# Kernel optimization log

Measured on AMD Instinct MI355X. Metric: run time of the kernel, lower is better.

## Reference

```python
import jax, jax.numpy as jnp
import numpy as np

B, C, H, W = 16, 3, 512, 512
TH, TW = 32, 32  # template h, w


def setup_inputs() -> dict:
    key = jax.random.key(0)
    k1, k2 = jax.random.split(key)
    im = jax.random.normal(k1, (B, C, H, W), dtype=jnp.float32)
    template = jax.random.normal(k2, (B, C, TH, TW), dtype=jnp.float32)
    return {"im": im, "template": template}


def _integral(x):
    # double cumsum -> integral image
    return jnp.cumsum(jnp.cumsum(x, axis=-1), axis=-2)


def _rect_sum(int_im, out_h, out_w, rh, rw):
    # Sum over rh x rw rectangles centered on each pixel. Because the gather
    # indices in the torch code form contiguous ranges, advanced indexing
    # reduces to 4 static slices of the integral image.
    return (int_im[..., :out_h, :out_w] + int_im[..., rh:, rw:]
            - int_im[..., :out_h, rw:] - int_im[..., rh:, :out_w])


def _ncc(im, template):
    Hh, Ww = im.shape[-2], im.shape[-1]
    th, tw = template.shape[-2], template.shape[-1]
    padWl = (tw - 1) // 2
    padWr = padWl + 1 - tw % 2
    padHt = (th - 1) // 2
    padHb = padHt + 1 - th % 2
    rh = padHt + padHb + 1  # rectangle height (== th for even th)
    rw = padWl + padWr + 1
    pad2d = ((0, 0), (0, 0), (padHt + 1, padHb), (padWl + 1, padWr))

    # local-mean centering via integral image
    rect = _rect_sum(_integral(jnp.pad(im, pad2d)), Hh, Ww, rh, rw)
    im_c = im - rect / (th * tw)
    t_c = template - template.mean(axis=(-2, -1), keepdims=True)

    # local energy via second integral image over squared centered image
    rect2 = _rect_sum(_integral(jnp.pad(im_c * im_c, pad2d)), Hh, Ww, rh, rw)
    energy = jnp.sqrt(jnp.clip(rect2, 0.0))
    t_norm = jnp.sqrt(jnp.sum(t_c * t_c, axis=(-2, -1), keepdims=True))

    # FFT cross-correlation (padding='same')
    ph = Hh + th - th % 2 - Hh % 2
    pw = Ww + tw - tw % 2 - Ww % 2
    f_im = jnp.fft.rfft2(im_c / energy, s=(ph, pw))
    f_t = jnp.fft.rfft2(jnp.flip(t_c / t_norm, axis=(-2, -1)), s=(ph, pw))
    full = jnp.fft.irfft2(f_im * f_t, s=(ph, pw))
    hH, hW = th // 2, tw // 2
    return full[..., hH:hH + Hh, hW:hW + Ww]


def reference(im, template):
    return _ncc(im, template)
```

## Files before the change

### kernel.cpp

```cpp
#include <hip/hip_runtime.h>
#include <hip/hip_bf16.h>
#include <math.h>

#define HH 512
#define WW 512
#define BC 48
#define GW 544
#define GH 545
#define PST (GH * GW)

#define ROWB 384
#define COPYSTRIDE 6208
#define BUFSTRIDE (2 * COPYSTRIDE)
#define LDSBYTES (2 * BUFSTRIDE)

#define SIMS 98

typedef __bf16 v8bf __attribute__((ext_vector_type(8)));
typedef float v16f __attribute__((ext_vector_type(16)));

__global__ __launch_bounds__(256) void k_template(const float* __restrict__ t,
                                                  __hip_bfloat16* __restrict__ tn)
{
    __shared__ float red[256];
    const int bc = blockIdx.x, tid = threadIdx.x;
    const float* tp = t + bc * 1024;
    float v0 = tp[tid], v1 = tp[tid + 256], v2 = tp[tid + 512], v3 = tp[tid + 768];
    red[tid] = v0 + v1 + v2 + v3;
    __syncthreads();
    for (int sft = 128; sft > 0; sft >>= 1) {
        if (tid < sft) red[tid] += red[tid + sft];
        __syncthreads();
    }
    float mean = red[0] * (1.0f / 1024.0f);
    __syncthreads();
    float c0 = v0 - mean, c1 = v1 - mean, c2 = v2 - mean, c3 = v3 - mean;
    red[tid] = c0 * c0 + c1 * c1 + c2 * c2 + c3 * c3;
    __syncthreads();
    for (int sft = 128; sft > 0; sft >>= 1) {
        if (tid < sft) red[tid] += red[tid + sft];
        __syncthreads();
    }
    float norm = sqrtf(red[0]);
    __hip_bfloat16* o = tn + bc * 1024;
    o[tid] = __float2bfloat16(c0 / norm);
    o[tid + 256] = __float2bfloat16(c1 / norm);
    o[tid + 512] = __float2bfloat16(c2 / norm);
    o[tid + 768] = __float2bfloat16(c3 / norm);
}

__global__ __launch_bounds__(256) void k_center2(const float* __restrict__ im,
                                                 __hip_bfloat16* __restrict__ T0)
{
    __shared__ __hip_bfloat16 sim[159 * SIMS];
    __shared__ float hs[159 * 64];
    const int j0 = blockIdx.x * 64;
    const int i0 = blockIdx.y * 128;
    const int plane = blockIdx.z;
    const int tid = threadIdx.x;
    const size_t iplane = (size_t)plane * HH * WW;
    const size_t gplane = (size_t)plane * PST;

    for (int k = tid; k < 159 * 96; k += 256) {
        int r = k / 96, c = k - r * 96;
        int gi = i0 + r - 15, gj = j0 + c - 16;
        float v = (gi >= 0 && gi < HH && gj >= 0 && gj < WW)
                      ? im[iplane + (size_t)gi * WW + gj] : 0.f;
        sim[r * SIMS + c] = __float2bfloat16(v);
    }
    __syncthreads();

    if (tid < 159) {
        const __hip_bfloat16* sr = sim + tid * SIMS;
        float s0 = 0.f;
#pragma unroll
        for (int c = 1; c <= 32; c++) s0 += __bfloat162float(sr[c]);
        hs[tid * 64] = s0;
        for (int j = 1; j < 64; j++) {
            s0 += __bfloat162float(sr[j + 32]) - __bfloat162float(sr[j]);
            hs[tid * 64 + j] = s0;
        }
    }
    __syncthreads();

    const int tc = tid & 63;
    const int lr0 = (tid >> 6) * 32;
    float run = 0.f;
#pragma unroll
    for (int d = 0; d < 32; d++) run += hs[(lr0 + d) * 64 + tc];
    for (int rr = 0; rr < 32; rr++) {
        int lr = lr0 + rr;
        int gi = i0 + lr;
        float imv = __bfloat162float(sim[(lr + 15) * SIMS + tc + 16]);
        float val = imv - run * (1.0f / 1024.0f);
        T0[gplane + (size_t)(16 + gi) * GW + 16 + j0 + tc] = __float2bfloat16(val);
        if (rr < 31) run += hs[(lr + 32) * 64 + tc] - hs[lr * 64 + tc];
    }
    if (blockIdx.x == 0) {
        for (int k = tid; k < 128 * 16; k += 256) {
            int rr = k >> 4, x = k & 15;
            T0[gplane + (size_t)(16 + i0 + rr) * GW + x] = __float2bfloat16(0.f);
        }
    }
    if (blockIdx.x == 7) {
        for (int k = tid; k < 128 * 16; k += 256) {
            int rr = k >> 4, x = k & 15;
            T0[gplane + (size_t)(16 + i0 + rr) * GW + 528 + x] = __float2bfloat16(0.f);
        }
    }
    if (blockIdx.x == 0 && blockIdx.y == 0) {
        for (int k = tid; k < 16 * GW; k += 256)
            T0[gplane + k] = __float2bfloat16(0.f);
    }
    if (blockIdx.x == 0 && blockIdx.y == 3) {
        size_t b = gplane + (size_t)528 * GW;
        for (int k = tid; k < 17 * GW; k += 256)
            T0[b + k] = __float2bfloat16(0.f);
    }
}

__global__ __launch_bounds__(256) void k_norm2(const __hip_bfloat16* __restrict__ T0,
                                               __hip_bfloat16* __restrict__ G0,
                                               __hip_bfloat16* __restrict__ G1)
{
    __shared__ __hip_bfloat16 sim[159 * SIMS];
    __shared__ float hs[159 * 64];
    const int j0 = blockIdx.x * 64;
    const int i0 = blockIdx.y * 128;
    const int plane = blockIdx.z;
    const int tid = threadIdx.x;
    const size_t gplane = (size_t)plane * PST;

    for (int k = tid; k < 159 * 96; k += 256) {
        int r = k / 96, c = k - r * 96;
        sim[r * SIMS + c] = T0[gplane + (size_t)(i0 + 1 + r) * GW + j0 + c];
    }
    __syncthreads();

    if (tid < 159) {
        const __hip_bfloat16* sr = sim + tid * SIMS;
        float s0 = 0.f;
#pragma unroll
        for (int c = 1; c <= 32; c++) {
            float v = __bfloat162float(sr[c]);
            s0 += v * v;
        }
        hs[tid * 64] = s0;
        for (int j = 1; j < 64; j++) {
            float a = __bfloat162float(sr[j + 32]);
            float b = __bfloat162float(sr[j]);
            s0 += a * a - b * b;
            hs[tid * 64 + j] = s0;
        }
    }
    __syncthreads();

    const int tc = tid & 63;
    const int lr0 = (tid >> 6) * 32;
    float run = 0.f;
#pragma unroll
    for (int d = 0; d < 32; d++) run += hs[(lr0 + d) * 64 + tc];
    for (int rr = 0; rr < 32; rr++) {
        int lr = lr0 + rr;
        int gi = i0 + lr;
        int c = j0 + tc;
        float e = sqrtf(fmaxf(run, 0.f));
        float v = __bfloat162float(sim[(lr + 15) * SIMS + tc + 16]) / e;
        __hip_bfloat16 w = __float2bfloat16(v);
        size_t pr = gplane + (size_t)(16 + gi) * GW;
        G0[pr + 16 + c] = w;
        G1[pr + 15 + c] = w;
        if (rr < 31) run += hs[(lr + 32) * 64 + tc] - hs[lr * 64 + tc];
    }
    if (blockIdx.x == 0) {
        for (int k = tid; k < 128 * 16; k += 256) {
            int rr = k >> 4, x = k & 15;
            size_t pr = gplane + (size_t)(16 + i0 + rr) * GW;
            G0[pr + x] = __float2bfloat16(0.f);
            if (x < 15) G1[pr + x] = __float2bfloat16(0.f);
        }
    }
    if (blockIdx.x == 7) {
        for (int k = tid; k < 128 * 17; k += 256) {
            int rr = k / 17, x = k % 17;
            size_t pr = gplane + (size_t)(16 + i0 + rr) * GW;
            G1[pr + 527 + x] = __float2bfloat16(0.f);
            if (x > 0) G0[pr + 527 + x] = __float2bfloat16(0.f);
        }
    }
    if (blockIdx.x == 0 && blockIdx.y == 0) {
        for (int k = tid; k < 16 * GW; k += 256) {
            G0[gplane + k] = __float2bfloat16(0.f);
            G1[gplane + k] = __float2bfloat16(0.f);
        }
    }
    if (blockIdx.x == 0 && blockIdx.y == 3) {
        size_t b = gplane + (size_t)528 * GW;
        for (int k = tid; k < 17 * GW; k += 256) {
            G0[b + k] = __float2bfloat16(0.f);
            G1[b + k] = __float2bfloat16(0.f);
        }
    }
}

template <int PHASE>
__device__ __forceinline__ void compute_chunk(const unsigned int* __restrict__ Lr,
                                              v8bf a0, v8bf a1,
                                              float (&C)[16],
                                              int h, int Tbase, int i0,
                                              float* outp)
{
#pragma unroll
    for (int t = 0; t < 16; ++t) {
        const unsigned int* p = Lr + PHASE * (BUFSTRIDE / 4) + t * (ROWB / 4);
        union { unsigned int u[4]; v8bf v; } B0, B1;
        B0.u[0] = p[0];  B0.u[1] = p[1];  B0.u[2] = p[2];  B0.u[3] = p[3];
        B1.u[0] = p[8];  B1.u[1] = p[9];  B1.u[2] = p[10]; B1.u[3] = p[11];
        v16f c;
#pragma unroll
        for (int q = 0; q < 16; ++q) c[q] = C[q];
        c = __builtin_amdgcn_mfma_f32_32x32x16_bf16(a1, B1.v, c, 0, 0, 0);
        c = __builtin_amdgcn_mfma_f32_32x32x16_bf16(a0, B0.v, c, 0, 0, 0);
        const int T = Tbase + t;
        if (T >= 31 && T <= 94) {
            if (h) {
                const int ret = i0 - 31 + T;
                outp[(size_t)ret * WW] = c[15];
            }
        }
        float t3  = __shfl_xor(c[3], 32);
        float t7  = __shfl_xor(c[7], 32);
        float t11 = __shfl_xor(c[11], 32);
        float t15 = __shfl_xor(c[15], 32);
        C[0]  = h ? t3  : 0.f;
        C[4]  = h ? t7  : t3;
        C[8]  = h ? t11 : t7;
        C[12] = h ? t15 : t11;
#pragma unroll
        for (int g = 0; g < 4; ++g)
#pragma unroll
            for (int k = 1; k < 4; ++k)
                C[4 * g + k] = c[4 * g + k - 1];
    }
}

__global__ __launch_bounds__(256) void k_corr_mfma(const __hip_bfloat16* __restrict__ G0,
                                                   const __hip_bfloat16* __restrict__ G1,
                                                   const __hip_bfloat16* __restrict__ Tn,
                                                   float* __restrict__ out)
{
    __shared__ __align__(16) char lds[LDSBYTES];
    const int tid = threadIdx.x;
    const int wid = tid >> 6;
    const int lane = tid & 63;
    const int n = lane & 31;
    const int h = lane >> 5;
    const int j0 = blockIdx.x * 128;
    const int j0w = j0 + wid * 32;
    const int i0 = blockIdx.y * 64;
    const int plane = blockIdx.z;

    const v8bf* tp = (const v8bf*)(Tn + (size_t)plane * 1024 + n * 32 + 8 * h);
    const v8bf a0 = tp[0];
    const v8bf a1 = tp[2];

    const int c0 = j0w + n - 15 + 8 * h;
    const int sel = c0 & 1;
    const int dbase = (32 * wid + n + 1 + 8 * h - sel) >> 1;
    const unsigned int* Lr = (const unsigned int*)(lds + sel * COPYSTRIDE) + dbase;

    const __hip_bfloat16* g0p = G0 + (size_t)plane * PST + (size_t)(i0 + 1) * GW + j0;
    const __hip_bfloat16* g1p = G1 + (size_t)plane * PST + (size_t)(i0 + 1) * GW + j0;

    const __hip_bfloat16* srcp[3];
    int ldso[3];
#pragma unroll
    for (int k = 0; k < 3; ++k) {
        int s = wid + 4 * k;
        int cp = (s >= 6) ? 1 : 0;
        int c2 = cp ? (s - 6) : s;
        int q = c2 * 1024 + lane * 16;
        int rl = q / ROWB;
        int cb = q - rl * ROWB;
        srcp[k] = (cp ? g1p : g0p) + rl * GW + (cb >> 1);
        ldso[k] = cp * COPYSTRIDE + c2 * 1024;
    }

    float C[16];
#pragma unroll
    for (int s = 0; s < 16; s++) C[s] = 0.f;

    float* outp = out + (size_t)plane * HH * WW + j0w + n;

    auto stage = [&](int R, int b) {
#pragma unroll
        for (int k = 0; k < 3; ++k) {
            __builtin_amdgcn_global_load_lds(
                (const __attribute__((address_space(1))) void*)(srcp[k] + (size_t)R * GW),
                (__attribute__((address_space(3))) void*)(lds + b * BUFSTRIDE + ldso[k]),
                16, 0, 0);
        }
    };

    stage(0, 0);
    stage(16, 1);
    __syncthreads();

    for (int k2 = 0; k2 < 3; ++k2) {
        compute_chunk<0>(Lr, a0, a1, C, h, 32 * k2, i0, outp);
        __syncthreads();
        if (k2 < 2) stage(32 * k2 + 32, 0);
        compute_chunk<1>(Lr, a0, a1, C, h, 32 * k2 + 16, i0, outp);
        __syncthreads();
        if (k2 < 2) stage(32 * k2 + 48, 1);
    }
}

extern "C" void kernel_launch(void* const* d_in, const int* in_sizes, int n_in,
                              void* d_out, int out_size, void* d_ws, size_t ws_size,
                              hipStream_t stream)
{
    const float* im = (const float*)d_in[0];
    const float* tmpl = (const float*)d_in[1];
    float* outp = (float*)d_out;
    __hip_bfloat16* T0 = (__hip_bfloat16*)d_out;
    __hip_bfloat16* G0 = (__hip_bfloat16*)d_ws;
    __hip_bfloat16* G1 = G0 + (size_t)BC * PST;
    __hip_bfloat16* Tn = G1 + (size_t)BC * PST;

    k_template<<<48, 256, 0, stream>>>(tmpl, Tn);
    k_center2<<<dim3(8, 4, BC), 256, 0, stream>>>(im, T0);
    k_norm2<<<dim3(8, 4, BC), 256, 0, stream>>>(T0, G0, G1);
    k_corr_mfma<<<dim3(4, 8, BC), 256, 0, stream>>>(G0, G1, Tn, outp);
}
```

Before: 299.7 us.

## Halve row tile and parallelize horizontal box sums in centering/norm kernels

The centering and energy-normalization kernels now process 64-row tiles instead of 128, doubling the grid. The horizontal sliding-window pass is split across four threads per row (16 columns each) instead of one serial thread per row. The hs buffer gets a padded stride of 65 to avoid LDS bank conflicts. The aim is to cut the serial horizontal-scan latency and raise occupancy. In exchange, the halo rows between tiles are reloaded more often (95 rows per 64 instead of 159 per 128), and each thread recomputes its initial 32-element window sum.

```diff
diff --git a/kernel.cpp b/kernel.cpp
--- a/kernel.cpp
+++ b/kernel.cpp
@@ -15,6 +15,7 @@
 #define LDSBYTES (2 * BUFSTRIDE)
 
 #define SIMS 98
+#define HSS 65
 
 typedef __bf16 v8bf __attribute__((ext_vector_type(8)));
 typedef float v16f __attribute__((ext_vector_type(16)));
@@ -52,16 +53,16 @@
 __global__ __launch_bounds__(256) void k_center2(const float* __restrict__ im,
                                                  __hip_bfloat16* __restrict__ T0)
 {
-    __shared__ __hip_bfloat16 sim[159 * SIMS];
-    __shared__ float hs[159 * 64];
+    __shared__ __hip_bfloat16 sim[95 * SIMS];
+    __shared__ float hs[95 * HSS];
     const int j0 = blockIdx.x * 64;
-    const int i0 = blockIdx.y * 128;
+    const int i0 = blockIdx.y * 64;
     const int plane = blockIdx.z;
     const int tid = threadIdx.x;
     const size_t iplane = (size_t)plane * HH * WW;
     const size_t gplane = (size_t)plane * PST;
 
-    for (int k = tid; k < 159 * 96; k += 256) {
+    for (int k = tid; k < 95 * 96; k += 256) {
         int r = k / 96, c = k - r * 96;
         int gi = i0 + r - 15, gj = j0 + c - 16;
         float v = (gi >= 0 && gi < HH && gj >= 0 && gj < WW)
@@ -70,40 +71,44 @@
     }
     __syncthreads();
 
-    if (tid < 159) {
-        const __hip_bfloat16* sr = sim + tid * SIMS;
-        float s0 = 0.f;
-#pragma unroll
-        for (int c = 1; c <= 32; c++) s0 += __bfloat162float(sr[c]);
-        hs[tid * 64] = s0;
-        for (int j = 1; j < 64; j++) {
-            s0 += __bfloat162float(sr[j + 32]) - __bfloat162float(sr[j]);
-            hs[tid * 64 + j] = s0;
+    for (int t = tid; t < 95 * 4; t += 256) {
+        const int r = t >> 2;
+        const int q = (t & 3) << 4;
+        const __hip_bfloat16* sr = sim + r * SIMS + q;
+        float s = 0.f;
+#pragma unroll
+        for (int c = 1; c <= 32; ++c) s += __bfloat162float(sr[c]);
+        float* hr = hs + r * HSS + q;
+        hr[0] = s;
+#pragma unroll
+        for (int j = 1; j < 16; ++j) {
+            s += __bfloat162float(sr[j + 32]) - __bfloat162float(sr[j]);
+            hr[j] = s;
         }
     }
     __syncthreads();
 
     const int tc = tid & 63;
-    const int lr0 = (tid >> 6) * 32;
+    const int lr0 = (tid >> 6) << 4;
     float run = 0.f;
 #pragma unroll
-    for (int d = 0; d < 32; d++) run += hs[(lr0 + d) * 64 + tc];
-    for (int rr = 0; rr < 32; rr++) {
-        int lr = lr0 + rr;
-        int gi = i0 + lr;
+    for (int d = 0; d < 32; ++d) run += hs[(lr0 + d) * HSS + tc];
+    for (int rr = 0; rr < 16; ++rr) {
+        const int lr = lr0 + rr;
         float imv = __bfloat162float(sim[(lr + 15) * SIMS + tc + 16]);
         float val = imv - run * (1.0f / 1024.0f);
-        T0[gplane + (size_t)(16 + gi) * GW + 16 + j0 + tc] = __float2bfloat16(val);
-        if (rr < 31) run += hs[(lr + 32) * 64 + tc] - hs[lr * 64 + tc];
-    }
+        T0[gplane + (size_t)(16 + i0 + lr) * GW + 16 + j0 + tc] = __float2bfloat16(val);
+        if (rr < 15) run += hs[(lr + 32) * HSS + tc] - hs[lr * HSS + tc];
+    }
+
     if (blockIdx.x == 0) {
-        for (int k = tid; k < 128 * 16; k += 256) {
+        for (int k = tid; k < 64 * 16; k += 256) {
             int rr = k >> 4, x = k & 15;
             T0[gplane + (size_t)(16 + i0 + rr) * GW + x] = __float2bfloat16(0.f);
         }
     }
     if (blockIdx.x == 7) {
-        for (int k = tid; k < 128 * 16; k += 256) {
+        for (int k = tid; k < 64 * 16; k += 256) {
             int rr = k >> 4, x = k & 15;
             T0[gplane + (size_t)(16 + i0 + rr) * GW + 528 + x] = __float2bfloat16(0.f);
         }
@@ -112,7 +117,7 @@
         for (int k = tid; k < 16 * GW; k += 256)
             T0[gplane + k] = __float2bfloat16(0.f);
     }
-    if (blockIdx.x == 0 && blockIdx.y == 3) {
+    if (blockIdx.x == 0 && blockIdx.y == 7) {
         size_t b = gplane + (size_t)528 * GW;
         for (int k = tid; k < 17 * GW; k += 256)
             T0[b + k] = __float2bfloat16(0.f);
@@ -123,57 +128,60 @@
                                                __hip_bfloat16* __restrict__ G0,
                                                __hip_bfloat16* __restrict__ G1)
 {
-    __shared__ __hip_bfloat16 sim[159 * SIMS];
-    __shared__ float hs[159 * 64];
+    __shared__ __hip_bfloat16 sim[95 * SIMS];
+    __shared__ float hs[95 * HSS];
     const int j0 = blockIdx.x * 64;
-    const int i0 = blockIdx.y * 128;
+    const int i0 = blockIdx.y * 64;
     const int plane = blockIdx.z;
     const int tid = threadIdx.x;
     const size_t gplane = (size_t)plane * PST;
 
-    for (int k = tid; k < 159 * 96; k += 256) {
+    for (int k = tid; k < 95 * 96; k += 256) {
         int r = k / 96, c = k - r * 96;
         sim[r * SIMS + c] = T0[gplane + (size_t)(i0 + 1 + r) * GW + j0 + c];
     }
     __syncthreads();
 
-    if (tid < 159) {
-        const __hip_bfloat16* sr = sim + tid * SIMS;
-        float s0 = 0.f;
-#pragma unroll
-        for (int c = 1; c <= 32; c++) {
+    for (int t = tid; t < 95 * 4; t += 256) {
+        const int r = t >> 2;
+        const int q = (t & 3) << 4;
+        const __hip_bfloat16* sr = sim + r * SIMS + q;
+        float s = 0.f;
+#pragma unroll
+        for (int c = 1; c <= 32; ++c) {
             float v = __bfloat162float(sr[c]);
-            s0 += v * v;
-        }
-        hs[tid * 64] = s0;
-        for (int j = 1; j < 64; j++) {
+            s += v * v;
+        }
+        float* hr = hs + r * HSS + q;
+        hr[0] = s;
+#pragma unroll
+        for (int j = 1; j < 16; ++j) {
             float a = __bfloat162float(sr[j + 32]);
             float b = __bfloat162float(sr[j]);
-            s0 += a * a - b * b;
-            hs[tid * 64 + j] = s0;
+            s += a * a - b * b;
+            hr[j] = s;
         }
     }
     __syncthreads();
 
     const int tc = tid & 63;
-    const int lr0 = (tid >> 6) * 32;
+    const int lr0 = (tid >> 6) << 4;
     float run = 0.f;
 #pragma unroll
-    for (int d = 0; d < 32; d++) run += hs[(lr0 + d) * 64 + tc];
-    for (int rr = 0; rr < 32; rr++) {
-        int lr = lr0 + rr;
-        int gi = i0 + lr;
-        int c = j0 + tc;
+    for (int d = 0; d < 32; ++d) run += hs[(lr0 + d) * HSS + tc];
+    for (int rr = 0; rr < 16; ++rr) {
+        const int lr = lr0 + rr;
         float e = sqrtf(fmaxf(run, 0.f));
         float v = __bfloat162float(sim[(lr + 15) * SIMS + tc + 16]) / e;
         __hip_bfloat16 w = __float2bfloat16(v);
-        size_t pr = gplane + (size_t)(16 + gi) * GW;
-        G0[pr + 16 + c] = w;
-        G1[pr + 15 + c] = w;
-        if (rr < 31) run += hs[(lr + 32) * 64 + tc] - hs[lr * 64 + tc];
-    }
+        size_t pr = gplane + (size_t)(16 + i0 + lr) * GW;
+        G0[pr + 16 + j0 + tc] = w;
+        G1[pr + 15 + j0 + tc] = w;
+        if (rr < 15) run += hs[(lr + 32) * HSS + tc] - hs[lr * HSS + tc];
+    }
+
     if (blockIdx.x == 0) {
-        for (int k = tid; k < 128 * 16; k += 256) {
+        for (int k = tid; k < 64 * 16; k += 256) {
             int rr = k >> 4, x = k & 15;
             size_t pr = gplane + (size_t)(16 + i0 + rr) * GW;
             G0[pr + x] = __float2bfloat16(0.f);
@@ -181,7 +189,7 @@
         }
     }
     if (blockIdx.x == 7) {
-        for (int k = tid; k < 128 * 17; k += 256) {
+        for (int k = tid; k < 64 * 17; k += 256) {
             int rr = k / 17, x = k % 17;
             size_t pr = gplane + (size_t)(16 + i0 + rr) * GW;
             G1[pr + 527 + x] = __float2bfloat16(0.f);
@@ -194,7 +202,7 @@
             G1[gplane + k] = __float2bfloat16(0.f);
         }
     }
-    if (blockIdx.x == 0 && blockIdx.y == 3) {
+    if (blockIdx.x == 0 && blockIdx.y == 7) {
         size_t b = gplane + (size_t)528 * GW;
         for (int k = tid; k < 17 * GW; k += 256) {
             G0[b + k] = __float2bfloat16(0.f);
@@ -329,7 +337,7 @@
     __hip_bfloat16* Tn = G1 + (size_t)BC * PST;
 
     k_template<<<48, 256, 0, stream>>>(tmpl, Tn);
-    k_center2<<<dim3(8, 4, BC), 256, 0, stream>>>(im, T0);
-    k_norm2<<<dim3(8, 4, BC), 256, 0, stream>>>(T0, G0, G1);
+    k_center2<<<dim3(8, 8, BC), 256, 0, stream>>>(im, T0);
+    k_norm2<<<dim3(8, 8, BC), 256, 0, stream>>>(T0, G0, G1);
     k_corr_mfma<<<dim3(4, 8, BC), 256, 0, stream>>>(G0, G1, Tn, outp);
 }
```

New measurement: 279.3 us. 6.8% less time.
